# Kernel optimization log

Hardware: AMD Instinct MI355X
Metric: run time of the kernel (lower is better)

The kernel has to match this reference:

```python
import jax, jax.numpy as jnp
import numpy as np


def setup_inputs() -> dict:
    key = jax.random.key(0)
    k1, k2, k3, k4, k5 = jax.random.split(key, 5)
    B, C, V, D, O = 8, 64, 25000, 12, 64
    x = jax.random.normal(k1, (B, C, V), dtype=jnp.float32)
    nbr_idx = jax.random.randint(k2, (B, V, D), 0, V, dtype=jnp.int32)
    # true 1-ring valence in [1, D]
    deg = jax.random.randint(k3, (B, V), 1, D + 1, dtype=jnp.int32)
    # conv weight [O, C, 1, 2] flattened to [O, C, 2], fan-in init scale
    W = jax.random.normal(k4, (O, C, 2), dtype=jnp.float32) * (1.0 / np.sqrt(C * 2))
    b = jax.random.normal(k5, (O,), dtype=jnp.float32) * 0.01
    return {"x": x, "nbr_idx": nbr_idx, "deg": deg, "W": W, "b": b}


def reference(x, nbr_idx, deg, W, b):
    # x: [B, C, V]; nbr_idx: [B, V, D] padded 1-ring; deg: [B, V] valid count
    B, C, V = x.shape
    D = nbr_idx.shape[-1]
    # gather neighbor features: [B, C, V, D]
    gathered = jax.vmap(lambda xb, ib: xb[:, ib])(x, nbr_idx)
    mask = (jnp.arange(D, dtype=deg.dtype)[None, None, :] < deg[:, :, None])  # [B, V, D]
    maskf = mask.astype(x.dtype)[:, None, :, :]  # [B, 1, V, D]
    denom = jnp.maximum(deg, 1).astype(x.dtype)[:, None, :]  # [B, 1, V]
    nbr_mean = jnp.sum(gathered * maskf, axis=-1) / denom  # [B, C, V]
    # G: [B, C, V, 2] = (self feature, 1-ring mean); conv2d kernel (1,2)
    G = jnp.stack([x, nbr_mean], axis=-1)
    out = jnp.einsum('bcvk,ock->bov', G, W) + b[None, :, None]
    return out[..., None]  # [B, O, V, 1]
```

## Files before the change

kernel.cpp:

```cpp
#include <hip/hip_runtime.h>
#include <stdint.h>


#define NB 8
#define NC 64
#define NV 25000
#define ND 12
#define NO 64
#define VROW 32
#define NGT 196
#define NTB 782
#define GTB 256

typedef uint32_t u32x4 __attribute__((ext_vector_type(4)));
typedef uint32_t u32x2 __attribute__((ext_vector_type(2)));
typedef __bf16  bf16x8 __attribute__((ext_vector_type(8)));
typedef float   f32x4  __attribute__((ext_vector_type(4)));

__device__ inline uint32_t bf16pack(float a, float b) {
    uint32_t ua = __float_as_uint(a), ub = __float_as_uint(b);
    ua = (ua + 0x7fffu + ((ua >> 16) & 1u)) >> 16;
    ub = (ub + 0x7fffu + ((ub >> 16) & 1u)) >> 16;
    return ua | (ub << 16);
}
__device__ inline float blo(uint32_t u) { return __uint_as_float(u << 16); }
__device__ inline float bhi(uint32_t u) { return __uint_as_float(u & 0xffff0000u); }

__global__ __launch_bounds__(256) void wt_kernel(const float* __restrict__ W,
                                                 uint32_t* __restrict__ Wcb) {
    int i = blockIdx.x * 256 + threadIdx.x;
    int m = i >> 5;
    int c = (i & 31) * 2;
    int k = m >> 6;
    int o = m & 63;
    float s0 = W[o * (NC * 2) + c * 2 + k];
    float s1 = W[o * (NC * 2) + (c + 1) * 2 + k];
    Wcb[i] = bf16pack(s0, s1);
}

__global__ __launch_bounds__(512, 4) void ygemm6(const float* __restrict__ x,
                                                 const uint32_t* __restrict__ Wcb,
                                                 const float* __restrict__ bias,
                                                 uint32_t* __restrict__ y0,
                                                 uint32_t* __restrict__ y1) {
    __shared__ uint32_t lb[4608 + 4096];
    uint32_t* yst0 = lb;
    uint32_t* yst1 = lb + 4608;

    const int b = blockIdx.x & 7;
    const int tile = blockIdx.x >> 3;
    const int vbase = tile * 128;
    const int t = threadIdx.x;
    const int lane = t & 63, wave = t >> 6;
    const float* xb = x + (size_t)b * NC * NV;

    {
        int vg = vbase + lane * 2;
        if (vg > NV - 2) vg = NV - 2;
        const int key = ((lane >> 1) & 7) << 2;
#pragma unroll
        for (int pp = 0; pp < 4; ++pp) {
            const int p = wave * 4 + pp;
            const int c = p * 2;
            u32x2 qa = __builtin_nontemporal_load(
                reinterpret_cast<const u32x2*>(xb + (size_t)c * NV + vg));
            u32x2 qb = __builtin_nontemporal_load(
                reinterpret_cast<const u32x2*>(xb + (size_t)(c + 1) * NV + vg));
            const int pc = p ^ key;
            lb[(lane * 2)     * 36 + pc] =
                bf16pack(__uint_as_float(qa[0]), __uint_as_float(qb[0]));
            lb[(lane * 2 + 1) * 36 + pc] =
                bf16pack(__uint_as_float(qa[1]), __uint_as_float(qb[1]));
        }
    }
    __syncthreads();

    const int l15 = lane & 15, lq = lane >> 4;
    const int pl = wave >> 2, sub = wave & 3;

    union BF { u32x4 q; bf16x8 v; } bfr[2][2];
#pragma unroll
    for (int s = 0; s < 2; ++s) {
        const int vl = sub * 32 + s * 16 + l15;
        const int key = ((vl >> 2) & 7) << 2;
#pragma unroll
        for (int kt = 0; kt < 2; ++kt)
            bfr[s][kt].q = *reinterpret_cast<const u32x4*>(
                &lb[vl * 36 + ((kt * 16 + lq * 4) ^ key)]);
    }
    __syncthreads();

    f32x4 acc[2][4];
#pragma unroll
    for (int s = 0; s < 2; ++s)
#pragma unroll
        for (int mt = 0; mt < 4; ++mt) acc[s][mt] = (f32x4){0.f, 0.f, 0.f, 0.f};

#pragma unroll
    for (int kt = 0; kt < 2; ++kt) {
#pragma unroll
        for (int mt = 0; mt < 4; ++mt) {
            union { u32x4 q; bf16x8 v; } au;
            au.q = *(const u32x4*)(Wcb + (size_t)(pl * 64 + mt * 16 + l15) * 32
                                       + kt * 16 + lq * 4);
#pragma unroll
            for (int s = 0; s < 2; ++s)
                acc[s][mt] = __builtin_amdgcn_mfma_f32_16x16x32_bf16(au.v, bfr[s][kt].v,
                                                                     acc[s][mt], 0, 0, 0);
        }
    }

    uint32_t* yst = pl ? yst1 : yst0;
#pragma unroll
    for (int s = 0; s < 2; ++s) {
        const int vrow = sub * 32 + s * 16 + l15;
        const int key = (vrow & 7) << 2;
#pragma unroll
        for (int mt = 0; mt < 4; ++mt) {
            f32x4 a = acc[s][mt];
            if (pl == 0) {
                const float* bp = bias + mt * 16 + lq * 4;
                a[0] += bp[0]; a[1] += bp[1]; a[2] += bp[2]; a[3] += bp[3];
            }
            u32x2 pk = {bf16pack(a[0], a[1]), bf16pack(a[2], a[3])};
            *reinterpret_cast<u32x2*>(&yst[vrow * 32 + ((mt * 8 + lq * 2) ^ key)]) = pk;
        }
    }
    __syncthreads();

    {
        uint32_t* y0g = y0 + ((size_t)b * NV + vbase) * VROW;
        uint32_t* y1g = y1 + ((size_t)b * NV + vbase) * VROW;
#pragma unroll
        for (int h = 0; h < 2; ++h) {
            const int ck = t + h * 512;
            const int r = ck >> 3;
            if (vbase + r < NV) {
                const int off = ((ck & 7) * 4) ^ ((r & 7) << 2);
                u32x4 q0 = *reinterpret_cast<const u32x4*>(&yst0[r * 32 + off]);
                __builtin_nontemporal_store(q0, reinterpret_cast<u32x4*>(y0g + ck * 4));
                u32x4 q1 = *reinterpret_cast<const u32x4*>(&yst1[r * 32 + off]);
                *reinterpret_cast<u32x4*>(y1g + ck * 4) = q1;
            }
        }
    }
}

__global__ __launch_bounds__(256) void gather3(const int* __restrict__ nbr,
                                               const int* __restrict__ deg,
                                               const uint32_t* __restrict__ y0,
                                               const uint32_t* __restrict__ y1,
                                               float* __restrict__ out) {
    __shared__ float lds[2][32 * 68];

    const int b = blockIdx.x & 7;
    const int t0 = blockIdx.x >> 3;
    const int lane = threadIdx.x & 63;
    const int wave = threadIdx.x >> 6;
    const int s8 = lane >> 3;
    const int j = lane & 7;
    const int vloc = wave * 8 + s8;

    const int* nbrb = nbr + (size_t)b * NV * ND;
    const int* degb = deg + (size_t)b * NV;
    const uint32_t* y0b = y0 + (size_t)b * NV * VROW;
    const uint32_t* y1b = y1 + (size_t)b * NV * VROW;
    float* outb = out + (size_t)b * NO * NV;

    int idx[ND];
    int dg;
    u32x4 su;
    {
        int v = t0 * 32 + vloc;
        const int vc = v < NV ? v : NV - 1;
        const int4* p = reinterpret_cast<const int4*>(nbrb + (size_t)vc * ND);
        int4 a0 = p[0], a1 = p[1], a2 = p[2];
        idx[0] = a0.x; idx[1] = a0.y; idx[2]  = a0.z; idx[3]  = a0.w;
        idx[4] = a1.x; idx[5] = a1.y; idx[6]  = a1.z; idx[7]  = a1.w;
        idx[8] = a2.x; idx[9] = a2.y; idx[10] = a2.z; idx[11] = a2.w;
        dg = degb[vc];
        su = *(reinterpret_cast<const u32x4*>(y0b + (size_t)vc * VROW) + j);
    }

    int buf = 0;
    for (int t = t0; t < NTB; t += GTB) {
        u32x4 rows[ND];
#pragma unroll
        for (int d = 0; d < ND; ++d) {
            if (d < dg)
                rows[d] = *(reinterpret_cast<const u32x4*>(
                                y1b + (size_t)idx[d] * VROW) + j);
        }

        const int tn = (t + GTB < NTB) ? t + GTB : t;
        int idxn[ND];
        int dgn;
        u32x4 sun;
        {
            int v = tn * 32 + vloc;
            const int vc = v < NV ? v : NV - 1;
            const int4* p = reinterpret_cast<const int4*>(nbrb + (size_t)vc * ND);
            int4 a0 = p[0], a1 = p[1], a2 = p[2];
            idxn[0] = a0.x; idxn[1] = a0.y; idxn[2]  = a0.z; idxn[3]  = a0.w;
            idxn[4] = a1.x; idxn[5] = a1.y; idxn[6]  = a1.z; idxn[7]  = a1.w;
            idxn[8] = a2.x; idxn[9] = a2.y; idxn[10] = a2.z; idxn[11] = a2.w;
            dgn = degb[vc];
            sun = *(reinterpret_cast<const u32x4*>(y0b + (size_t)vc * VROW) + j);
        }

        const float inv = 1.0f / (float)dg;
        float ns[8];
#pragma unroll
        for (int k = 0; k < 8; ++k) ns[k] = 0.0f;
#pragma unroll
        for (int d = 0; d < ND; ++d) {
            if (d < dg) {
                u32x4 u = rows[d];
                ns[0] += blo(u[0]); ns[1] += bhi(u[0]);
                ns[2] += blo(u[1]); ns[3] += bhi(u[1]);
                ns[4] += blo(u[2]); ns[5] += bhi(u[2]);
                ns[6] += blo(u[3]); ns[7] += bhi(u[3]);
            }
        }

        {
            float f[8];
            f[0] = __builtin_fmaf(inv, ns[0], blo(su[0]));
            f[1] = __builtin_fmaf(inv, ns[1], bhi(su[0]));
            f[2] = __builtin_fmaf(inv, ns[2], blo(su[1]));
            f[3] = __builtin_fmaf(inv, ns[3], bhi(su[1]));
            f[4] = __builtin_fmaf(inv, ns[4], blo(su[2]));
            f[5] = __builtin_fmaf(inv, ns[5], bhi(su[2]));
            f[6] = __builtin_fmaf(inv, ns[6], blo(su[3]));
            f[7] = __builtin_fmaf(inv, ns[7], bhi(su[3]));
            f32x4 w0 = {f[0], f[1], f[2], f[3]};
            f32x4 w1 = {f[4], f[5], f[6], f[7]};
            *reinterpret_cast<f32x4*>(&lds[buf][vloc * 68 + j * 8])     = w0;
            *reinterpret_cast<f32x4*>(&lds[buf][vloc * 68 + j * 8 + 4]) = w1;
        }
        __syncthreads();

        {
            const int vl = threadIdx.x & 31;
            const int o8 = threadIdx.x >> 5;
            const int vv = t * 32 + vl;
            if (vv < NV) {
#pragma unroll
                for (int oo = 0; oo < 8; ++oo) {
                    const int o = oo * 8 + o8;
                    __builtin_nontemporal_store(lds[buf][vl * 68 + o],
                                                outb + (size_t)o * NV + vv);
                }
            }
        }

        buf ^= 1;
        dg = dgn;
        su = sun;
#pragma unroll
        for (int d = 0; d < ND; ++d) idx[d] = idxn[d];
    }
}

__global__ __launch_bounds__(64) void fallback_kernel(const float* __restrict__ x,
                                                      const int* __restrict__ nbr,
                                                      const int* __restrict__ deg,
                                                      const float* __restrict__ W,
                                                      const float* __restrict__ bias,
                                                      float* __restrict__ out) {
    const int bvi = blockIdx.x;
    const int b = bvi / NV, v = bvi % NV;
    const int o = threadIdx.x;
    const int degv = deg[bvi];
    const float inv = 1.0f / (float)degv;
    float acc = bias[o];
    for (int c = 0; c < NC; ++c) {
        const float* xc = x + ((size_t)b * NC + c) * NV;
        float m = 0.0f;
        for (int d = 0; d < degv; ++d) m += xc[nbr[(size_t)bvi * ND + d]];
        acc += W[o * (NC * 2) + c * 2] * xc[v] + W[o * (NC * 2) + c * 2 + 1] * (m * inv);
    }
    out[((size_t)b * NO + o) * NV + v] = acc;
}

extern "C" void kernel_launch(void* const* d_in, const int* in_sizes, int n_in,
                              void* d_out, int out_size, void* d_ws, size_t ws_size,
                              hipStream_t stream) {
    const float* x    = (const float*)d_in[0];
    const int*   nbr  = (const int*)d_in[1];
    const int*   deg  = (const int*)d_in[2];
    const float* W    = (const float*)d_in[3];
    const float* bias = (const float*)d_in[4];
    float* out = (float*)d_out;

    const size_t wcb_dw = 4096;
    const size_t plane  = (size_t)NB * NV * VROW;
    const size_t need = (wcb_dw + 2 * plane) * 4;
    if (ws_size >= need) {
        uint32_t* Wcb = (uint32_t*)d_ws;
        uint32_t* y0  = Wcb + wcb_dw;
        uint32_t* y1  = y0 + plane;
        wt_kernel<<<dim3(16), 256, 0, stream>>>(W, Wcb);
        ygemm6<<<dim3(NB * NGT), 512, 0, stream>>>(x, Wcb, bias, y0, y1);
        gather3<<<dim3(NB * GTB), 256, 0, stream>>>(nbr, deg, y0, y1, out);
    } else {
        fallback_kernel<<<dim3(NB * NV), 64, 0, stream>>>(x, nbr, deg, W, bias, out);
    }
}
```

Before: 168.6 us.

## Replace persistent prefetching gather with one-tile-per-block 512-thread gather

The gather kernel's persistent grid-stride loop with software prefetch of the next tile's indices is replaced by a kernel that launches one block per 32-vertex tile. Each block has 512 threads and each vertex is served by 16 lanes loading 8-byte bf16 chunks instead of 8 lanes loading 16-byte chunks. The aim is more memory-level parallelism and occupancy to hide the latency of the random neighbour reads. The cost is smaller, less coalesced gather loads, the loss of cross-tile prefetch, and more block launches. The self-feature read now uses a nontemporal load.

```diff
diff --git a/kernel.cpp b/kernel.cpp
--- a/kernel.cpp
+++ b/kernel.cpp
@@ -9,8 +9,7 @@
 #define NO 64
 #define VROW 32
 #define NGT 196
-#define NTB 782
-#define GTB 256
+#define GVT 782
 
 typedef uint32_t u32x4 __attribute__((ext_vector_type(4)));
 typedef uint32_t u32x2 __attribute__((ext_vector_type(2)));
@@ -146,119 +145,80 @@
     }
 }
 
-__global__ __launch_bounds__(256) void gather3(const int* __restrict__ nbr,
-                                               const int* __restrict__ deg,
-                                               const uint32_t* __restrict__ y0,
-                                               const uint32_t* __restrict__ y1,
-                                               float* __restrict__ out) {
-    __shared__ float lds[2][32 * 68];
+__global__ __launch_bounds__(512, 4) void gather5(const int* __restrict__ nbr,
+                                                  const int* __restrict__ deg,
+                                                  const uint32_t* __restrict__ y0,
+                                                  const uint32_t* __restrict__ y1,
+                                                  float* __restrict__ out) {
+    __shared__ float lds[32 * 68];
 
     const int b = blockIdx.x & 7;
-    const int t0 = blockIdx.x >> 3;
-    const int lane = threadIdx.x & 63;
-    const int wave = threadIdx.x >> 6;
-    const int s8 = lane >> 3;
-    const int j = lane & 7;
-    const int vloc = wave * 8 + s8;
-
-    const int* nbrb = nbr + (size_t)b * NV * ND;
-    const int* degb = deg + (size_t)b * NV;
-    const uint32_t* y0b = y0 + (size_t)b * NV * VROW;
+    const int tile = blockIdx.x >> 3;
+    const int t = threadIdx.x;
+    const int vloc = t >> 4;
+    const int sl = t & 15;
+    const int v = tile * 32 + vloc;
+    const int vc = v < NV ? v : NV - 1;
+    const size_t bv = (size_t)b * NV + vc;
+
     const uint32_t* y1b = y1 + (size_t)b * NV * VROW;
-    float* outb = out + (size_t)b * NO * NV;
+
+    u32x2 su = __builtin_nontemporal_load(
+        reinterpret_cast<const u32x2*>(y0 + bv * VROW) + sl);
 
     int idx[ND];
-    int dg;
-    u32x4 su;
-    {
-        int v = t0 * 32 + vloc;
-        const int vc = v < NV ? v : NV - 1;
-        const int4* p = reinterpret_cast<const int4*>(nbrb + (size_t)vc * ND);
+    {
+        const int4* p = reinterpret_cast<const int4*>(nbr + bv * ND);
         int4 a0 = p[0], a1 = p[1], a2 = p[2];
         idx[0] = a0.x; idx[1] = a0.y; idx[2]  = a0.z; idx[3]  = a0.w;
         idx[4] = a1.x; idx[5] = a1.y; idx[6]  = a1.z; idx[7]  = a1.w;
         idx[8] = a2.x; idx[9] = a2.y; idx[10] = a2.z; idx[11] = a2.w;
-        dg = degb[vc];
-        su = *(reinterpret_cast<const u32x4*>(y0b + (size_t)vc * VROW) + j);
-    }
-
-    int buf = 0;
-    for (int t = t0; t < NTB; t += GTB) {
-        u32x4 rows[ND];
-#pragma unroll
-        for (int d = 0; d < ND; ++d) {
-            if (d < dg)
-                rows[d] = *(reinterpret_cast<const u32x4*>(
-                                y1b + (size_t)idx[d] * VROW) + j);
-        }
-
-        const int tn = (t + GTB < NTB) ? t + GTB : t;
-        int idxn[ND];
-        int dgn;
-        u32x4 sun;
-        {
-            int v = tn * 32 + vloc;
-            const int vc = v < NV ? v : NV - 1;
-            const int4* p = reinterpret_cast<const int4*>(nbrb + (size_t)vc * ND);
-            int4 a0 = p[0], a1 = p[1], a2 = p[2];
-            idxn[0] = a0.x; idxn[1] = a0.y; idxn[2]  = a0.z; idxn[3]  = a0.w;
-            idxn[4] = a1.x; idxn[5] = a1.y; idxn[6]  = a1.z; idxn[7]  = a1.w;
-            idxn[8] = a2.x; idxn[9] = a2.y; idxn[10] = a2.z; idxn[11] = a2.w;
-            dgn = degb[vc];
-            sun = *(reinterpret_cast<const u32x4*>(y0b + (size_t)vc * VROW) + j);
-        }
-
-        const float inv = 1.0f / (float)dg;
-        float ns[8];
-#pragma unroll
-        for (int k = 0; k < 8; ++k) ns[k] = 0.0f;
-#pragma unroll
-        for (int d = 0; d < ND; ++d) {
-            if (d < dg) {
-                u32x4 u = rows[d];
-                ns[0] += blo(u[0]); ns[1] += bhi(u[0]);
-                ns[2] += blo(u[1]); ns[3] += bhi(u[1]);
-                ns[4] += blo(u[2]); ns[5] += bhi(u[2]);
-                ns[6] += blo(u[3]); ns[7] += bhi(u[3]);
+    }
+    const int dg = deg[bv];
+    const float inv = 1.0f / (float)dg;
+
+    u32x2 rows[ND];
+#pragma unroll
+    for (int d = 0; d < ND; ++d) {
+        if (d < dg)
+            rows[d] = *(reinterpret_cast<const u32x2*>(
+                            y1b + (size_t)idx[d] * VROW) + sl);
+    }
+
+    float ns[4];
+#pragma unroll
+    for (int k = 0; k < 4; ++k) ns[k] = 0.0f;
+#pragma unroll
+    for (int d = 0; d < ND; ++d) {
+        if (d < dg) {
+            u32x2 u = rows[d];
+            ns[0] += blo(u[0]); ns[1] += bhi(u[0]);
+            ns[2] += blo(u[1]); ns[3] += bhi(u[1]);
+        }
+    }
+
+    {
+        f32x4 w;
+        w[0] = __builtin_fmaf(inv, ns[0], blo(su[0]));
+        w[1] = __builtin_fmaf(inv, ns[1], bhi(su[0]));
+        w[2] = __builtin_fmaf(inv, ns[2], blo(su[1]));
+        w[3] = __builtin_fmaf(inv, ns[3], bhi(su[1]));
+        *reinterpret_cast<f32x4*>(&lds[vloc * 68 + sl * 4]) = w;
+    }
+    __syncthreads();
+
+    {
+        const int vl = t & 31;
+        const int o8 = t >> 5;
+        const int vv = tile * 32 + vl;
+        if (vv < NV) {
+            float* ob = out + (size_t)b * NO * NV + vv;
+#pragma unroll
+            for (int oo = 0; oo < 4; ++oo) {
+                const int o = oo * 16 + o8;
+                __builtin_nontemporal_store(lds[vl * 68 + o], ob + (size_t)o * NV);
             }
         }
-
-        {
-            float f[8];
-            f[0] = __builtin_fmaf(inv, ns[0], blo(su[0]));
-            f[1] = __builtin_fmaf(inv, ns[1], bhi(su[0]));
-            f[2] = __builtin_fmaf(inv, ns[2], blo(su[1]));
-            f[3] = __builtin_fmaf(inv, ns[3], bhi(su[1]));
-            f[4] = __builtin_fmaf(inv, ns[4], blo(su[2]));
-            f[5] = __builtin_fmaf(inv, ns[5], bhi(su[2]));
-            f[6] = __builtin_fmaf(inv, ns[6], blo(su[3]));
-            f[7] = __builtin_fmaf(inv, ns[7], bhi(su[3]));
-            f32x4 w0 = {f[0], f[1], f[2], f[3]};
-            f32x4 w1 = {f[4], f[5], f[6], f[7]};
-            *reinterpret_cast<f32x4*>(&lds[buf][vloc * 68 + j * 8])     = w0;
-            *reinterpret_cast<f32x4*>(&lds[buf][vloc * 68 + j * 8 + 4]) = w1;
-        }
-        __syncthreads();
-
-        {
-            const int vl = threadIdx.x & 31;
-            const int o8 = threadIdx.x >> 5;
-            const int vv = t * 32 + vl;
-            if (vv < NV) {
-#pragma unroll
-                for (int oo = 0; oo < 8; ++oo) {
-                    const int o = oo * 8 + o8;
-                    __builtin_nontemporal_store(lds[buf][vl * 68 + o],
-                                                outb + (size_t)o * NV + vv);
-                }
-            }
-        }
-
-        buf ^= 1;
-        dg = dgn;
-        su = sun;
-#pragma unroll
-        for (int d = 0; d < ND; ++d) idx[d] = idxn[d];
     }
 }
 
@@ -302,7 +262,7 @@
         uint32_t* y1  = y0 + plane;
         wt_kernel<<<dim3(16), 256, 0, stream>>>(W, Wcb);
         ygemm6<<<dim3(NB * NGT), 512, 0, stream>>>(x, Wcb, bias, y0, y1);
-        gather3<<<dim3(NB * GTB), 256, 0, stream>>>(nbr, deg, y0, y1, out);
+        gather5<<<dim3(NB * GVT), 512, 0, stream>>>(nbr, deg, y0, y1, out);
     } else {
         fallback_kernel<<<dim3(NB * NV), 64, 0, stream>>>(x, nbr, deg, W, bias, out);
     }
```

Measured after the change: 171.2 us. About the same (+1.5%).
